# Kernel optimization log

Measured on AMD Instinct MI355X. Metric: run time of the kernel, lower is better.

## Reference

```python
import jax, jax.numpy as jnp
import numpy as np

S, B, D, H, F, E = 2048, 8, 512, 8, 2048, 64
CAP_FACTOR = 2
EPS = 1e-5


def setup_inputs() -> dict:
    key = jax.random.key(0)
    ks = jax.random.split(key, 12)
    s = 0.02
    return {
        "src": jax.random.normal(ks[0], (S, B, D), jnp.float32),
        "in_proj_w": jax.random.normal(ks[1], (3 * D, D), jnp.float32) * s,
        "in_proj_b": jnp.zeros((3 * D,), jnp.float32),
        "out_proj_w": jax.random.normal(ks[2], (D, D), jnp.float32) * s,
        "out_proj_b": jnp.zeros((D,), jnp.float32),
        "ln1_g": jnp.ones((D,), jnp.float32),
        "ln1_b": jnp.zeros((D,), jnp.float32),
        "gate_w": jax.random.normal(ks[3], (D, E), jnp.float32) * s,
        "w1": jax.random.normal(ks[4], (E, D, F), jnp.float32) * s,
        "b1": jnp.zeros((E, F), jnp.float32),
        "w2": jax.random.normal(ks[5], (E, F, D), jnp.float32) * s,
        "b2": jnp.zeros((E, D), jnp.float32),
        "ln2_g": jnp.ones((D,), jnp.float32),
        "ln2_b": jnp.zeros((D,), jnp.float32),
    }


def _layer_norm(x, g, b):
    mu = jnp.mean(x, -1, keepdims=True)
    var = jnp.mean(jnp.square(x - mu), -1, keepdims=True)
    return (x - mu) * jax.lax.rsqrt(var + EPS) * g + b


def reference(src, in_proj_w, in_proj_b, out_proj_w, out_proj_b,
              ln1_g, ln1_b, gate_w, w1, b1, w2, b2, ln2_g, ln2_b):
    hd = D // H
    # --- self attention (seq-first, as nn.MultiheadAttention) ---
    qkv = src @ in_proj_w.T + in_proj_b            # [S,B,3D]
    q, k, v = jnp.split(qkv, 3, axis=-1)
    q = q.reshape(S, B, H, hd)
    k = k.reshape(S, B, H, hd)
    v = v.reshape(S, B, H, hd)
    scores = jnp.einsum('qbhd,kbhd->bhqk', q, k) * (hd ** -0.5)
    attn = jax.nn.softmax(scores, axis=-1)
    ctx = jnp.einsum('bhqk,kbhd->qbhd', attn, v).reshape(S, B, D)
    attn_out = ctx @ out_proj_w.T + out_proj_b
    x = _layer_norm(src + attn_out, ln1_g, ln1_b)

    # --- MoE: top-1 gating + capacity dispatch + merged expert FFN ---
    N = S * B
    C = CAP_FACTOR * N // E                         # per-expert capacity
    xt = x.reshape(N, D)
    probs = jax.nn.softmax(xt @ gate_w, axis=-1)    # [N,E]
    eidx = jnp.argmax(probs, axis=-1)               # [N]
    gval = jnp.take_along_axis(probs, eidx[:, None], 1)[:, 0]
    onehot = jax.nn.one_hot(eidx, E, dtype=jnp.int32)
    pos = jnp.take_along_axis(jnp.cumsum(onehot, 0), eidx[:, None], 1)[:, 0] - 1
    pos_s = jnp.where(pos < C, pos, C)              # overflow tokens -> dummy slot C
    buf = jnp.zeros((E, C + 1, D), xt.dtype).at[eidx, pos_s].set(xt)
    xe = buf[:, :C]                                 # [E,C,D]
    h = jax.nn.relu(jnp.einsum('ecd,edf->ecf', xe, w1) + b1[:, None, :])
    ye = jnp.einsum('ecf,efd->ecd', h, w2) + b2[:, None, :]
    ye = jnp.pad(ye, ((0, 0), (0, 1), (0, 0)))      # slot C = zeros (dropped)
    yt = ye[eidx, pos_s] * gval[:, None]            # combine with gate weight
    moe_out = yt.reshape(S, B, D)

    return _layer_norm(x + moe_out, ln2_g, ln2_b)
```

## Files before the change

kernel.cpp:

```cpp
#include <hip/hip_runtime.h>
#include <hip/hip_bf16.h>

typedef __bf16 bf16_t;
typedef __bf16 bf16x8 __attribute__((ext_vector_type(8)));
typedef float f32x4 __attribute__((ext_vector_type(4)));

static constexpr int S_ = 2048;
static constexpr int B_ = 8;
static constexpr int D_ = 512;
static constexpr int H_ = 8;
static constexpr int HD_ = 64;
static constexpr int F_ = 2048;
static constexpr int E_ = 64;
static constexpr int NT = S_ * B_;
static constexpr int CAP = 512;
static constexpr float EPS_ = 1e-5f;

__device__ __forceinline__ float wave_sum(float v) {
#pragma unroll
  for (int m = 1; m < 64; m <<= 1) v += __shfl_xor(v, m);
  return v;
}

__device__ __forceinline__ void gload_lds16(const void* g, void* l) {
  __builtin_amdgcn_global_load_lds((const __attribute__((address_space(1))) void*)g,
                                   (__attribute__((address_space(3))) void*)l, 16, 0, 0);
}

__global__ void k_cvt(const float* __restrict__ in, bf16_t* __restrict__ out, int n8) {
  int i = blockIdx.x * blockDim.x + threadIdx.x;
  if (i >= n8) return;
  const float4* p = (const float4*)in + (size_t)i * 2;
  float4 a = p[0], b = p[1];
  bf16x8 o;
  o[0]=(bf16_t)a.x; o[1]=(bf16_t)a.y; o[2]=(bf16_t)a.z; o[3]=(bf16_t)a.w;
  o[4]=(bf16_t)b.x; o[5]=(bf16_t)b.y; o[6]=(bf16_t)b.z; o[7]=(bf16_t)b.w;
  ((bf16x8*)out)[i] = o;
}

__global__ void k_tcvt(const float* __restrict__ in, bf16_t* __restrict__ out,
                       int R, int C, long strideIn, long strideOut) {
  __shared__ __align__(16) float t[64][68];
  const float* ip = in + (long)blockIdx.z * strideIn;
  bf16_t* op = out + (long)blockIdx.z * strideOut;
  int r0 = blockIdx.y * 64, c0 = blockIdx.x * 64;
  int tid = threadIdx.x;
  int row = tid >> 2, cc = (tid & 3) * 16;
  const float4* g = (const float4*)(ip + (long)(r0 + row) * C + c0 + cc);
  float4 a0 = g[0], a1 = g[1], a2 = g[2], a3 = g[3];
  *(float4*)&t[row][cc + 0]  = a0;
  *(float4*)&t[row][cc + 4]  = a1;
  *(float4*)&t[row][cc + 8]  = a2;
  *(float4*)&t[row][cc + 12] = a3;
  __syncthreads();
  int oc = tid >> 2, rr = (tid & 3) * 16;
  bf16x8 o0, o1;
#pragma unroll
  for (int j = 0; j < 8; j++) o0[j] = (bf16_t)t[rr + j][oc];
#pragma unroll
  for (int j = 0; j < 8; j++) o1[j] = (bf16_t)t[rr + 8 + j][oc];
  *(bf16x8*)(op + (long)(c0 + oc) * R + r0 + rr)     = o0;
  *(bf16x8*)(op + (long)(c0 + oc) * R + r0 + rr + 8) = o1;
}

__global__ void k_tv(const bf16_t* __restrict__ qkv, bf16_t* __restrict__ vT) {
  __shared__ __align__(16) bf16_t t[64][72];
  int bh = blockIdx.y, bI = bh >> 3, hI = bh & 7;
  int s0 = blockIdx.x * 64;
  int tid = threadIdx.x;
  int row = tid >> 2, cc = (tid & 3) * 16;
  const uint4* g = (const uint4*)(qkv + ((long)(s0 + row) * B_ + bI) * 1536 + 1024 + hI * 64 + cc);
  uint4 v0 = g[0], v1 = g[1];
  *(uint4*)&t[row][cc]     = v0;
  *(uint4*)&t[row][cc + 8] = v1;
  __syncthreads();
  int oc = tid >> 2, rr = (tid & 3) * 16;
  bf16x8 o0, o1;
#pragma unroll
  for (int j = 0; j < 8; j++) o0[j] = t[rr + j][oc];
#pragma unroll
  for (int j = 0; j < 8; j++) o1[j] = t[rr + 8 + j][oc];
  bf16_t* op = vT + ((long)bh * 64 + oc) * (long)S_ + s0 + rr;
  *(bf16x8*)(op)     = o0;
  *(bf16x8*)(op + 8) = o1;
}

template <int RELU>
__global__ __launch_bounds__(256) void k_gemm(
    const bf16_t* __restrict__ A, const bf16_t* __restrict__ Bm,
    const float* __restrict__ bias, bf16_t* __restrict__ Cout,
    int K, int lda, int ldb, int ldc,
    long aStride, long bStride, long cStride, int biasStride,
    const int* __restrict__ cnt, int mCap) {
  __shared__ __align__(16) bf16_t As[128 * 32];
  __shared__ __align__(16) bf16_t Bs[128 * 32];
  int z = blockIdx.z;
  if (cnt) {
    int c = cnt[z]; if (c > mCap) c = mCap;
    if ((int)blockIdx.y * 128 >= c) return;
  }
  long m0 = (long)blockIdx.y * 128, n0 = (long)blockIdx.x * 128;
  const bf16_t* Ab = A + (long)z * aStride + m0 * lda;
  const bf16_t* Bb = Bm + (long)z * bStride + n0 * ldb;
  int tid = threadIdx.x, wid = tid >> 6, lane = tid & 63;
  int lr = lane & 15, lg = lane >> 4;
  int wm = wid >> 1, wn = wid & 1;
  int grow = wid * 16 + (lane >> 2);
  int gcol = (lane & 3) * 8;
  const bf16_t* gA0 = Ab + (long)grow * lda + gcol;
  const bf16_t* gA1 = gA0 + (long)64 * lda;
  const bf16_t* gB0 = Bb + (long)grow * ldb + gcol;
  const bf16_t* gB1 = gB0 + (long)64 * ldb;
  bf16_t* lA0 = &As[wid * 512 + lane * 8];
  bf16_t* lA1 = lA0 + 2048;
  bf16_t* lB0 = &Bs[wid * 512 + lane * 8];
  bf16_t* lB1 = lB0 + 2048;
  f32x4 acc[4][4] = {};
  for (int k0 = 0; k0 < K; k0 += 32) {
    gload_lds16(gA0 + k0, lA0);
    gload_lds16(gA1 + k0, lA1);
    gload_lds16(gB0 + k0, lB0);
    gload_lds16(gB1 + k0, lB1);
    __syncthreads();
    bf16x8 af[4], bfr[4];
#pragma unroll
    for (int i = 0; i < 4; i++) {
      af[i]  = *(const bf16x8*)&As[(wm * 64 + i * 16 + lr) * 32 + lg * 8];
      bfr[i] = *(const bf16x8*)&Bs[(wn * 64 + i * 16 + lr) * 32 + lg * 8];
    }
#pragma unroll
    for (int i = 0; i < 4; i++)
#pragma unroll
      for (int j = 0; j < 4; j++)
        acc[i][j] = __builtin_amdgcn_mfma_f32_16x16x32_bf16(af[i], bfr[j], acc[i][j], 0, 0, 0);
    __syncthreads();
  }
#pragma unroll
  for (int j = 0; j < 4; j++) {
    int col = (int)n0 + wn * 64 + j * 16 + lr;
    float bv = bias[(long)z * biasStride + col];
#pragma unroll
    for (int i = 0; i < 4; i++) {
      long row = m0 + wm * 64 + i * 16 + lg * 4;
#pragma unroll
      for (int r = 0; r < 4; r++) {
        float v = acc[i][j][r] + bv;
        if (RELU) v = fmaxf(v, 0.0f);
        Cout[(long)z * cStride + (row + r) * ldc + col] = (bf16_t)v;
      }
    }
  }
}

__global__ __launch_bounds__(256) void k_attn(const bf16_t* __restrict__ qkv,
                                              const bf16_t* __restrict__ vT,
                                              bf16_t* __restrict__ ctx) {
  constexpr int LP = 72;
  __shared__ __align__(16) bf16_t Kld[64 * LP];
  __shared__ __align__(16) bf16_t Vld[64 * LP];
  __shared__ __align__(16) bf16_t Pld[4][16 * LP];
  int bh = blockIdx.y, bI = bh >> 3, hI = bh & 7;
  int q0 = blockIdx.x * 64;
  int tid = threadIdx.x, wid = tid >> 6, lane = tid & 63;
  int lr = lane & 15, lg = lane >> 4;
  int qrow = q0 + wid * 16 + lr;
  const bf16_t* qb = qkv + ((long)qrow * B_ + bI) * 1536 + hI * 64;
  bf16x8 qf0 = *(const bf16x8*)(qb + lg * 8);
  bf16x8 qf1 = *(const bf16x8*)(qb + 32 + lg * 8);
  f32x4 o[4] = {};
  float mrun[4], lrun[4];
#pragma unroll
  for (int r = 0; r < 4; r++) { mrun[r] = -3.0e38f; lrun[r] = 0.0f; }
  const float SC = 0.125f * 1.44269504f;
  int srow = tid >> 2, sc = (tid & 3) * 16;
  for (int kb = 0; kb < S_ / 64; kb++) {
    int krow = kb * 64 + srow;
    const uint4* kg = (const uint4*)(qkv + ((long)krow * B_ + bI) * 1536 + 512 + hI * 64 + sc);
    const uint4* vg = (const uint4*)(vT + ((long)bh * 64 + srow) * (long)S_ + kb * 64 + sc);
    uint4 k0v = kg[0], k1v = kg[1], v0v = vg[0], v1v = vg[1];
    __syncthreads();
    *(uint4*)&Kld[srow * LP + sc]     = k0v;
    *(uint4*)&Kld[srow * LP + sc + 8] = k1v;
    *(uint4*)&Vld[srow * LP + sc]     = v0v;
    *(uint4*)&Vld[srow * LP + sc + 8] = v1v;
    __syncthreads();
    f32x4 sacc[4] = {};
#pragma unroll
    for (int kc = 0; kc < 2; kc++) {
      bf16x8 qf = kc ? qf1 : qf0;
#pragma unroll
      for (int kt = 0; kt < 4; kt++) {
        bf16x8 kf = *(const bf16x8*)&Kld[(kt * 16 + lr) * LP + kc * 32 + lg * 8];
        sacc[kt] = __builtin_amdgcn_mfma_f32_16x16x32_bf16(qf, kf, sacc[kt], 0, 0, 0);
      }
    }
#pragma unroll
    for (int kt = 0; kt < 4; kt++) sacc[kt] *= SC;
    float pv[4][4];
#pragma unroll
    for (int r = 0; r < 4; r++) {
      float mx = fmaxf(fmaxf(sacc[0][r], sacc[1][r]), fmaxf(sacc[2][r], sacc[3][r]));
      mx = fmaxf(mx, __shfl_xor(mx, 1));
      mx = fmaxf(mx, __shfl_xor(mx, 2));
      mx = fmaxf(mx, __shfl_xor(mx, 4));
      mx = fmaxf(mx, __shfl_xor(mx, 8));
      if (__any(mx > mrun[r] + 8.0f)) {
        float mnew = fmaxf(mrun[r], mx);
        float corr = exp2f(mrun[r] - mnew);
        lrun[r] *= corr;
#pragma unroll
        for (int nt = 0; nt < 4; nt++) o[nt][r] *= corr;
        mrun[r] = mnew;
      }
      float ps = 0.0f;
#pragma unroll
      for (int kt = 0; kt < 4; kt++) {
        float p = exp2f(sacc[kt][r] - mrun[r]);
        pv[kt][r] = p; ps += p;
      }
      ps += __shfl_xor(ps, 1); ps += __shfl_xor(ps, 2);
      ps += __shfl_xor(ps, 4); ps += __shfl_xor(ps, 8);
      lrun[r] += ps;
    }
#pragma unroll
    for (int kt = 0; kt < 4; kt++)
#pragma unroll
      for (int r = 0; r < 4; r++)
        Pld[wid][(lg * 4 + r) * LP + kt * 16 + lr] = (bf16_t)pv[kt][r];
#pragma unroll
    for (int ks = 0; ks < 2; ks++) {
      bf16x8 pa = *(const bf16x8*)&Pld[wid][lr * LP + ks * 32 + lg * 8];
#pragma unroll
      for (int nt = 0; nt < 4; nt++) {
        bf16x8 vb = *(const bf16x8*)&Vld[(nt * 16 + lr) * LP + ks * 32 + lg * 8];
        o[nt] = __builtin_amdgcn_mfma_f32_16x16x32_bf16(pa, vb, o[nt], 0, 0, 0);
      }
    }
  }
#pragma unroll
  for (int nt = 0; nt < 4; nt++)
#pragma unroll
    for (int r = 0; r < 4; r++) {
      int qr = q0 + wid * 16 + lg * 4 + r;
      float val = o[nt][r] / lrun[r];
      ctx[((long)qr * B_ + bI) * (long)D_ + hI * 64 + nt * 16 + lr] = (bf16_t)val;
    }
}

__global__ void k_ln_res(const float* __restrict__ base, const bf16_t* __restrict__ addb,
                         const float* __restrict__ g, const float* __restrict__ b,
                         float* __restrict__ out) {
  int w = (int)((blockIdx.x * blockDim.x + threadIdx.x) >> 6);
  int lane = threadIdx.x & 63;
  if (w >= NT) return;
  long off = (long)w * D_ + lane * 8;
  const float4* pb = (const float4*)(base + off);
  float4 b0 = pb[0], b1 = pb[1];
  bf16x8 av = *(const bf16x8*)(addb + off);
  float t[8];
  t[0]=b0.x+(float)av[0]; t[1]=b0.y+(float)av[1]; t[2]=b0.z+(float)av[2]; t[3]=b0.w+(float)av[3];
  t[4]=b1.x+(float)av[4]; t[5]=b1.y+(float)av[5]; t[6]=b1.z+(float)av[6]; t[7]=b1.w+(float)av[7];
  float s = t[0]+t[1]+t[2]+t[3]+t[4]+t[5]+t[6]+t[7];
  s = wave_sum(s);
  float mu = s * (1.0f / D_);
  float vv = 0.0f;
#pragma unroll
  for (int j = 0; j < 8; j++) { float d = t[j] - mu; vv += d * d; }
  vv = wave_sum(vv);
  float rstd = rsqrtf(vv * (1.0f / D_) + EPS_);
  const float4* pg = (const float4*)(g + lane * 8);
  const float4* pq = (const float4*)(b + lane * 8);
  float4 g0 = pg[0], g1 = pg[1], q0 = pq[0], q1 = pq[1];
  float4 o0, o1;
  o0.x=(t[0]-mu)*rstd*g0.x+q0.x; o0.y=(t[1]-mu)*rstd*g0.y+q0.y;
  o0.z=(t[2]-mu)*rstd*g0.z+q0.z; o0.w=(t[3]-mu)*rstd*g0.w+q0.w;
  o1.x=(t[4]-mu)*rstd*g1.x+q1.x; o1.y=(t[5]-mu)*rstd*g1.y+q1.y;
  o1.z=(t[6]-mu)*rstd*g1.z+q1.z; o1.w=(t[7]-mu)*rstd*g1.w+q1.w;
  float4* po = (float4*)(out + off);
  po[0] = o0; po[1] = o1;
}

__global__ void k_gate(const float* __restrict__ x, const float* __restrict__ gw,
                       int* __restrict__ eidx, float* __restrict__ gval) {
  int w = (int)((blockIdx.x * blockDim.x + threadIdx.x) >> 6);
  int lane = threadIdx.x & 63;
  if (w >= NT) return;
  const float* xr = x + (long)w * D_;
  float a0 = 0.0f, a1 = 0.0f, a2 = 0.0f, a3 = 0.0f;
#pragma unroll 4
  for (int k = 0; k < D_; k += 4) {
    a0 = fmaf(xr[k + 0], gw[(k + 0) * E_ + lane], a0);
    a1 = fmaf(xr[k + 1], gw[(k + 1) * E_ + lane], a1);
    a2 = fmaf(xr[k + 2], gw[(k + 2) * E_ + lane], a2);
    a3 = fmaf(xr[k + 3], gw[(k + 3) * E_ + lane], a3);
  }
  float acc = (a0 + a1) + (a2 + a3);
  float v = acc; int idx = lane;
#pragma unroll
  for (int m = 1; m < 64; m <<= 1) {
    float ov = __shfl_xor(v, m);
    int oi = __shfl_xor(idx, m);
    if (ov > v || (ov == v && oi < idx)) { v = ov; idx = oi; }
  }
  float s = __expf(acc - v);
  s = wave_sum(s);
  if (lane == 0) { eidx[w] = idx; gval[w] = 1.0f / s; }
}

__global__ void k_route(const float* __restrict__ x, const int* __restrict__ eidx,
                        int* __restrict__ pos, int* __restrict__ cnt,
                        bf16_t* __restrict__ xe) {
  int w = (int)((blockIdx.x * blockDim.x + threadIdx.x) >> 6);
  int lane = threadIdx.x & 63;
  if (w >= NT) return;
  int e = eidx[w];
  int p = 0;
  if (lane == 0) p = atomicAdd(&cnt[e], 1);
  p = __shfl(p, 0);
  if (lane == 0) pos[w] = p;
  if (p < CAP) {
    const float4* px = (const float4*)(x + (long)w * D_ + lane * 8);
    float4 a = px[0], b = px[1];
    bf16x8 o;
    o[0]=(bf16_t)a.x; o[1]=(bf16_t)a.y; o[2]=(bf16_t)a.z; o[3]=(bf16_t)a.w;
    o[4]=(bf16_t)b.x; o[5]=(bf16_t)b.y; o[6]=(bf16_t)b.z; o[7]=(bf16_t)b.w;
    *(bf16x8*)(xe + ((long)e * CAP + p) * D_ + lane * 8) = o;
  }
}

__global__ void k_final(const float* __restrict__ x, const bf16_t* __restrict__ ye,
                        const int* __restrict__ eidx, const int* __restrict__ pos,
                        const float* __restrict__ gval,
                        const float* __restrict__ g, const float* __restrict__ b,
                        float* __restrict__ out) {
  int w = (int)((blockIdx.x * blockDim.x + threadIdx.x) >> 6);
  int lane = threadIdx.x & 63;
  if (w >= NT) return;
  int e = eidx[w], p = pos[w];
  float gv = gval[w];
  long off = (long)w * D_ + lane * 8;
  const float4* px = (const float4*)(x + off);
  float4 x0 = px[0], x1 = px[1];
  float t[8] = {x0.x, x0.y, x0.z, x0.w, x1.x, x1.y, x1.z, x1.w};
  if (p < CAP) {
    bf16x8 yv = *(const bf16x8*)(ye + ((long)e * CAP + p) * D_ + lane * 8);
#pragma unroll
    for (int j = 0; j < 8; j++) t[j] += (float)yv[j] * gv;
  }
  float s = t[0]+t[1]+t[2]+t[3]+t[4]+t[5]+t[6]+t[7];
  s = wave_sum(s);
  float mu = s * (1.0f / D_);
  float vv = 0.0f;
#pragma unroll
  for (int j = 0; j < 8; j++) { float d = t[j] - mu; vv += d * d; }
  vv = wave_sum(vv);
  float rstd = rsqrtf(vv * (1.0f / D_) + EPS_);
  const float4* pg = (const float4*)(g + lane * 8);
  const float4* pq = (const float4*)(b + lane * 8);
  float4 g0 = pg[0], g1 = pg[1], q0 = pq[0], q1 = pq[1];
  float4 o0, o1;
  o0.x=(t[0]-mu)*rstd*g0.x+q0.x; o0.y=(t[1]-mu)*rstd*g0.y+q0.y;
  o0.z=(t[2]-mu)*rstd*g0.z+q0.z; o0.w=(t[3]-mu)*rstd*g0.w+q0.w;
  o1.x=(t[4]-mu)*rstd*g1.x+q1.x; o1.y=(t[5]-mu)*rstd*g1.y+q1.y;
  o1.z=(t[6]-mu)*rstd*g1.z+q1.z; o1.w=(t[7]-mu)*rstd*g1.w+q1.w;
  float4* po = (float4*)(out + off);
  po[0] = o0; po[1] = o1;
}

extern "C" void kernel_launch(void* const* d_in, const int* in_sizes, int n_in,
                              void* d_out, int out_size, void* d_ws, size_t ws_size,
                              hipStream_t stream) {
  const float* src        = (const float*)d_in[0];
  const float* in_proj_w  = (const float*)d_in[1];
  const float* in_proj_b  = (const float*)d_in[2];
  const float* out_proj_w = (const float*)d_in[3];
  const float* out_proj_b = (const float*)d_in[4];
  const float* ln1_g      = (const float*)d_in[5];
  const float* ln1_b      = (const float*)d_in[6];
  const float* gate_w     = (const float*)d_in[7];
  const float* w1         = (const float*)d_in[8];
  const float* b1         = (const float*)d_in[9];
  const float* w2         = (const float*)d_in[10];
  const float* b2         = (const float*)d_in[11];
  const float* ln2_g      = (const float*)d_in[12];
  const float* ln2_b      = (const float*)d_in[13];
  (void)in_sizes; (void)n_in; (void)out_size; (void)ws_size;

  char* ws = (char*)d_ws;
  size_t off = 0;
  auto alloc = [&](size_t bytes) -> char* {
    char* p = ws + off; off += (bytes + 255) & ~(size_t)255; return p;
  };
  bf16_t* src_bf  = (bf16_t*)alloc((size_t)NT * D_ * 2);
  bf16_t* w_in_bf = (bf16_t*)alloc((size_t)3 * D_ * D_ * 2);
  bf16_t* w_out_bf= (bf16_t*)alloc((size_t)D_ * D_ * 2);
  bf16_t* qkv_bf  = (bf16_t*)alloc((size_t)NT * 3 * D_ * 2);
  bf16_t* vT      = (bf16_t*)alloc((size_t)B_ * H_ * HD_ * S_ * 2);
  bf16_t* ctx_bf  = (bf16_t*)alloc((size_t)NT * D_ * 2);
  bf16_t* ao_bf   = (bf16_t*)alloc((size_t)NT * D_ * 2);
  float*  x_f32   = (float*)alloc((size_t)NT * D_ * 4);
  bf16_t* w1t     = (bf16_t*)alloc((size_t)E_ * D_ * F_ * 2);
  bf16_t* w2t     = (bf16_t*)alloc((size_t)E_ * F_ * D_ * 2);
  bf16_t* xe      = (bf16_t*)alloc((size_t)E_ * CAP * D_ * 2);
  bf16_t* hbuf    = (bf16_t*)alloc((size_t)E_ * CAP * F_ * 2);
  bf16_t* ye      = (bf16_t*)alloc((size_t)E_ * CAP * D_ * 2);
  int*    eidx    = (int*)alloc((size_t)NT * 4);
  int*    pos     = (int*)alloc((size_t)NT * 4);
  float*  gval    = (float*)alloc((size_t)NT * 4);
  int*    cnt     = (int*)alloc((size_t)E_ * 4);

  k_cvt<<<NT * D_ / 8 / 256, 256, 0, stream>>>(src, src_bf, NT * D_ / 8);
  k_cvt<<<3 * D_ * D_ / 8 / 256, 256, 0, stream>>>(in_proj_w, w_in_bf, 3 * D_ * D_ / 8);
  k_cvt<<<D_ * D_ / 8 / 256, 256, 0, stream>>>(out_proj_w, w_out_bf, D_ * D_ / 8);
  k_tcvt<<<dim3(F_ / 64, D_ / 64, E_), 256, 0, stream>>>(w1, w1t, D_, F_, (long)D_ * F_, (long)D_ * F_);
  k_tcvt<<<dim3(D_ / 64, F_ / 64, E_), 256, 0, stream>>>(w2, w2t, F_, D_, (long)F_ * D_, (long)F_ * D_);

  k_gemm<0><<<dim3(12, 128, 1), 256, 0, stream>>>(src_bf, w_in_bf, in_proj_b, qkv_bf,
      512, 512, 512, 1536, 0, 0, 0, 0, nullptr, NT);

  k_tv<<<dim3(S_ / 64, B_ * H_), 256, 0, stream>>>(qkv_bf, vT);
  k_attn<<<dim3(S_ / 64, B_ * H_), 256, 0, stream>>>(qkv_bf, vT, ctx_bf);
  k_gemm<0><<<dim3(4, 128, 1), 256, 0, stream>>>(ctx_bf, w_out_bf, out_proj_b, ao_bf,
      512, 512, 512, 512, 0, 0, 0, 0, nullptr, NT);
  k_ln_res<<<NT / 4, 256, 0, stream>>>(src, ao_bf, ln1_g, ln1_b, x_f32);

  k_gate<<<NT / 4, 256, 0, stream>>>(x_f32, gate_w, eidx, gval);
  hipMemsetAsync(cnt, 0, E_ * 4, stream);
  hipMemsetAsync(xe, 0, (size_t)E_ * CAP * D_ * 2, stream);
  k_route<<<NT / 4, 256, 0, stream>>>(x_f32, eidx, pos, cnt, xe);

  k_gemm<1><<<dim3(F_ / 128, CAP / 128, E_), 256, 0, stream>>>(xe, w1t, b1, hbuf,
      512, 512, 512, 2048, (long)CAP * D_, (long)F_ * D_, (long)CAP * F_, F_, cnt, CAP);
  k_gemm<0><<<dim3(D_ / 128, CAP / 128, E_), 256, 0, stream>>>(hbuf, w2t, b2, ye,
      2048, 2048, 2048, 512, (long)CAP * F_, (long)F_ * D_, (long)CAP * D_, D_, cnt, CAP);

  k_final<<<NT / 4, 256, 0, stream>>>(x_f32, ye, eidx, pos, gval, ln2_g, ln2_b, (float*)d_out);
}
```

Baseline: 1.421 ms.

## Compute transposed scores in attention and pass P via cross-lane shuffles instead of LDS

The QK^T MFMA operands are swapped so each lane holds all scores of one query column, which makes the row max and row sum nearly lane-local and needs only two cross-lane shuffles. The probabilities are packed to bf16 pairs and rearranged into the PV MFMA A-operand layout with register shuffles, removing the per-wave P staging buffer in shared memory and its write/read round trip. The lazy-rescale threshold is dropped, so the correction factor is applied on every block, and the K/V LDS pitch changes from 72 to 80. It trades LDS traffic for more shuffle instructions, and the shuffle layout mapping is easy to get wrong.

```diff
diff --git a/kernel.cpp b/kernel.cpp
--- a/kernel.cpp
+++ b/kernel.cpp
@@ -25,6 +25,12 @@
 __device__ __forceinline__ void gload_lds16(const void* g, void* l) {
   __builtin_amdgcn_global_load_lds((const __attribute__((address_space(1))) void*)g,
                                    (__attribute__((address_space(3))) void*)l, 16, 0, 0);
+}
+
+__device__ __forceinline__ unsigned pack2bf(float lo, float hi) {
+  union { bf16_t h; unsigned short u; } a, b;
+  a.h = (bf16_t)lo; b.h = (bf16_t)hi;
+  return ((unsigned)b.u << 16) | (unsigned)a.u;
 }
 
 __global__ void k_cvt(const float* __restrict__ in, bf16_t* __restrict__ out, int n8) {
@@ -155,10 +161,9 @@
 __global__ __launch_bounds__(256) void k_attn(const bf16_t* __restrict__ qkv,
                                               const bf16_t* __restrict__ vT,
                                               bf16_t* __restrict__ ctx) {
-  constexpr int LP = 72;
+  constexpr int LP = 80;
   __shared__ __align__(16) bf16_t Kld[64 * LP];
   __shared__ __align__(16) bf16_t Vld[64 * LP];
-  __shared__ __align__(16) bf16_t Pld[4][16 * LP];
   int bh = blockIdx.y, bI = bh >> 3, hI = bh & 7;
   int q0 = blockIdx.x * 64;
   int tid = threadIdx.x, wid = tid >> 6, lane = tid & 63;
@@ -168,10 +173,10 @@
   bf16x8 qf0 = *(const bf16x8*)(qb + lg * 8);
   bf16x8 qf1 = *(const bf16x8*)(qb + 32 + lg * 8);
   f32x4 o[4] = {};
-  float mrun[4], lrun[4];
-#pragma unroll
-  for (int r = 0; r < 4; r++) { mrun[r] = -3.0e38f; lrun[r] = 0.0f; }
+  float mrun = -3.0e38f, lrun = 0.0f;
   const float SC = 0.125f * 1.44269504f;
+  int s0sh = lr + ((lane & 16) ? 32 : 0);
+  int hi = lg >> 1;
   int srow = tid >> 2, sc = (tid & 3) * 16;
   for (int kb = 0; kb < S_ / 64; kb++) {
     int krow = kb * 64 + srow;
@@ -191,58 +196,75 @@
 #pragma unroll
       for (int kt = 0; kt < 4; kt++) {
         bf16x8 kf = *(const bf16x8*)&Kld[(kt * 16 + lr) * LP + kc * 32 + lg * 8];
-        sacc[kt] = __builtin_amdgcn_mfma_f32_16x16x32_bf16(qf, kf, sacc[kt], 0, 0, 0);
+        sacc[kt] = __builtin_amdgcn_mfma_f32_16x16x32_bf16(kf, qf, sacc[kt], 0, 0, 0);
       }
     }
 #pragma unroll
     for (int kt = 0; kt < 4; kt++) sacc[kt] *= SC;
-    float pv[4][4];
-#pragma unroll
-    for (int r = 0; r < 4; r++) {
-      float mx = fmaxf(fmaxf(sacc[0][r], sacc[1][r]), fmaxf(sacc[2][r], sacc[3][r]));
-      mx = fmaxf(mx, __shfl_xor(mx, 1));
-      mx = fmaxf(mx, __shfl_xor(mx, 2));
-      mx = fmaxf(mx, __shfl_xor(mx, 4));
-      mx = fmaxf(mx, __shfl_xor(mx, 8));
-      if (__any(mx > mrun[r] + 8.0f)) {
-        float mnew = fmaxf(mrun[r], mx);
-        float corr = exp2f(mrun[r] - mnew);
-        lrun[r] *= corr;
-#pragma unroll
-        for (int nt = 0; nt < 4; nt++) o[nt][r] *= corr;
-        mrun[r] = mnew;
+    float mx = -3.0e38f;
+#pragma unroll
+    for (int kt = 0; kt < 4; kt++)
+#pragma unroll
+      for (int r = 0; r < 4; r++) mx = fmaxf(mx, sacc[kt][r]);
+    mx = fmaxf(mx, __shfl_xor(mx, 16));
+    mx = fmaxf(mx, __shfl_xor(mx, 32));
+    float mnew = fmaxf(mrun, mx);
+    float corr = exp2f(mrun - mnew);
+    mrun = mnew;
+    float ps = 0.0f;
+    unsigned pk[8];
+#pragma unroll
+    for (int kt = 0; kt < 4; kt++) {
+      float p0 = exp2f(sacc[kt][0] - mnew);
+      float p1 = exp2f(sacc[kt][1] - mnew);
+      float p2 = exp2f(sacc[kt][2] - mnew);
+      float p3 = exp2f(sacc[kt][3] - mnew);
+      ps += (p0 + p1) + (p2 + p3);
+      pk[kt * 2]     = pack2bf(p0, p1);
+      pk[kt * 2 + 1] = pack2bf(p2, p3);
+    }
+    ps += __shfl_xor(ps, 16);
+    ps += __shfl_xor(ps, 32);
+    lrun = lrun * corr + ps;
+    float cr[4];
+#pragma unroll
+    for (int r = 0; r < 4; r++) cr[r] = __shfl(corr, lg * 4 + r);
+#pragma unroll
+    for (int nt = 0; nt < 4; nt++)
+#pragma unroll
+      for (int r = 0; r < 4; r++) o[nt][r] *= cr[r];
+#pragma unroll
+    for (int ks = 0; ks < 2; ks++) {
+      unsigned w[4];
+#pragma unroll
+      for (int h = 0; h < 2; h++) {
+        unsigned vA = pk[4 * ks + h];
+        unsigned vB = pk[4 * ks + 2 + h];
+        unsigned a0 = (unsigned)__shfl((int)vA, s0sh);
+        unsigned a1 = (unsigned)__shfl((int)vA, s0sh + 16);
+        unsigned b0 = (unsigned)__shfl((int)vB, s0sh);
+        unsigned b1 = (unsigned)__shfl((int)vB, s0sh + 16);
+        w[h]     = hi ? b0 : a0;
+        w[2 + h] = hi ? b1 : a1;
       }
-      float ps = 0.0f;
-#pragma unroll
-      for (int kt = 0; kt < 4; kt++) {
-        float p = exp2f(sacc[kt][r] - mrun[r]);
-        pv[kt][r] = p; ps += p;
-      }
-      ps += __shfl_xor(ps, 1); ps += __shfl_xor(ps, 2);
-      ps += __shfl_xor(ps, 4); ps += __shfl_xor(ps, 8);
-      lrun[r] += ps;
-    }
-#pragma unroll
-    for (int kt = 0; kt < 4; kt++)
-#pragma unroll
-      for (int r = 0; r < 4; r++)
-        Pld[wid][(lg * 4 + r) * LP + kt * 16 + lr] = (bf16_t)pv[kt][r];
-#pragma unroll
-    for (int ks = 0; ks < 2; ks++) {
-      bf16x8 pa = *(const bf16x8*)&Pld[wid][lr * LP + ks * 32 + lg * 8];
+      union { unsigned u[4]; bf16x8 v; } pw;
+      pw.u[0] = w[0]; pw.u[1] = w[1]; pw.u[2] = w[2]; pw.u[3] = w[3];
 #pragma unroll
       for (int nt = 0; nt < 4; nt++) {
         bf16x8 vb = *(const bf16x8*)&Vld[(nt * 16 + lr) * LP + ks * 32 + lg * 8];
-        o[nt] = __builtin_amdgcn_mfma_f32_16x16x32_bf16(pa, vb, o[nt], 0, 0, 0);
+        o[nt] = __builtin_amdgcn_mfma_f32_16x16x32_bf16(pw.v, vb, o[nt], 0, 0, 0);
       }
     }
   }
+  float lr4[4];
+#pragma unroll
+  for (int r = 0; r < 4; r++) lr4[r] = __shfl(lrun, lg * 4 + r);
 #pragma unroll
   for (int nt = 0; nt < 4; nt++)
 #pragma unroll
     for (int r = 0; r < 4; r++) {
       int qr = q0 + wid * 16 + lg * 4 + r;
-      float val = o[nt][r] / lrun[r];
+      float val = o[nt][r] / lr4[r];
       ctx[((long)qr * B_ + bI) * (long)D_ + hI * 64 + nt * 16 + lr] = (bf16_t)val;
     }
 }
```

Result: faster. 1.338 ms (-5.8%).
